# Kernel tuning notes

Hardware: AMD Instinct MI355X
Metric: run time of the kernel (lower is better)

Reference implementation:

```python
import jax, jax.numpy as jnp
import numpy as np

N = 4_194_304   # collocation points
H = 10          # num_neurons
L = 10          # num_layers (residual blocks)
DIN = 3         # (x, y, z) coords
DOUT = 1        # traveltime


def _linear_params(k, fan_in, fan_out, batch=()):
    # matches torch.nn.Linear default init: U(-1/sqrt(fan_in), 1/sqrt(fan_in))
    kw, kb = jax.random.split(k)
    s = 1.0 / np.sqrt(fan_in)
    W = jax.random.uniform(kw, batch + (fan_in, fan_out), minval=-s, maxval=s, dtype=jnp.float32)
    b = jax.random.uniform(kb, batch + (fan_out,), minval=-s, maxval=s, dtype=jnp.float32)
    return W, b


def setup_inputs() -> dict:
    key = jax.random.key(0)
    ks = jax.random.split(key, 8)
    x = jax.random.normal(ks[0], (N, DIN), dtype=jnp.float32)
    w0, b0 = _linear_params(ks[1], DIN, H)
    w1, b1 = _linear_params(ks[2], H, H)
    Wr1, Br1 = _linear_params(ks[3], H, H, (L,))
    Wr2, Br2 = _linear_params(ks[4], H, H, (L,))
    Wr3, Br3 = _linear_params(ks[5], H, H, (L,))
    w8, b8 = _linear_params(ks[6], H, H)
    w9, b9 = _linear_params(ks[7], H, DOUT)
    return dict(x=x, w0=w0, b0=b0, w1=w1, b1=b1,
                Wr1=Wr1, Br1=Br1, Wr2=Wr2, Br2=Br2, Wr3=Wr3, Br3=Br3,
                w8=w8, b8=b8, w9=w9, b9=b9)


def reference(x, w0, b0, w1, b1, Wr1, Br1, Wr2, Br2, Wr3, Br3, w8, b8, w9, b9):
    relu = jax.nn.relu
    h = relu(x @ w0 + b0)          # [N, H]
    h = relu(h @ w1 + b1)          # [N, H]

    def block(h, params):
        W1, B1, W2, B2, W3, B3 = params
        h1 = relu(h @ W1 + B1)
        h2 = relu(h1 @ W3 + B3 + h @ W2 + B2)  # residual mixing of x0 via W2
        return h2, None

    h, _ = jax.lax.scan(block, h, (Wr1, Br1, Wr2, Br2, Wr3, Br3))
    h = relu(h @ w8 + b8)
    out = h @ w9 + b9              # last_act=None, last_abs=False, last_multiplier=1
    return out
```

## Files before the change

### kernel.cpp

```cpp
#include <hip/hip_runtime.h>


#define NPTS 4194304
#define NBLK 2048
#define WPB 4
#define NWAVES (NBLK * WPB)
#define NTILES (NPTS / 32)
#define TPW (NTILES / NWAVES)
#define NMM 24
#define NLDS 20
#define ILP 2

typedef _Float16 h8 __attribute__((ext_vector_type(8)));
typedef float v16f __attribute__((ext_vector_type(16)));
typedef unsigned u4v __attribute__((ext_vector_type(4)));

__device__ __forceinline__ v16f mm(h8 a, h8 b, v16f c) {
    return __builtin_amdgcn_mfma_f32_32x32x16_f16(a, b, c, 0, 0, 0);
}
__device__ __forceinline__ unsigned pkrtz(float a, float b) {
    return __builtin_bit_cast(unsigned, __builtin_amdgcn_cvt_pkrtz(a, b));
}
__device__ __forceinline__ h8 relu8(h8 h) {
    h8 z = {0, 0, 0, 0, 0, 0, 0, 0};
    return __builtin_elementwise_max(h, z);
}
__device__ __forceinline__ h8 rc_lo(v16f d) {
    u4v u;
    u.x = pkrtz(d[0], d[1]); u.y = pkrtz(d[2], d[3]);
    u.z = pkrtz(d[4], d[5]); u.w = pkrtz(d[6], d[7]);
    return relu8(__builtin_bit_cast(h8, u));
}
__device__ __forceinline__ h8 rc_hi(v16f d) {
    u4v u;
    u.x = pkrtz(d[8], d[9]);   u.y = pkrtz(d[10], d[11]);
    u.z = pkrtz(d[12], d[13]); u.w = pkrtz(d[14], d[15]);
    return relu8(__builtin_bit_cast(h8, u));
}

__global__ __launch_bounds__(64) void prepack(
    const float* __restrict__ w0, const float* __restrict__ b0,
    const float* __restrict__ w1, const float* __restrict__ b1,
    const float* __restrict__ Wr1, const float* __restrict__ Br1,
    const float* __restrict__ Wr2, const float* __restrict__ Br2,
    const float* __restrict__ Wr3, const float* __restrict__ Br3,
    const float* __restrict__ w8, const float* __restrict__ b8,
    const float* __restrict__ w9, const float* __restrict__ b9,
    h8* __restrict__ tab)
{
    const int q = blockIdx.x, l = threadIdx.x;
    const int m = l & 31, g = l >> 5;
    h8 v;
#pragma unroll
    for (int j = 0; j < 8; ++j) {
        const int rr = (j & 3) + 8 * (j >> 2) + 4 * g;
        float a = 0.0f;
        if (q == 0) {
            if (m < 10 && rr < 3)        a = w0[rr * 10 + m];
            else if (m < 10 && rr == 3)  a = b0[m];
            else if (m == 10 && rr == 3) a = 1.0f;
        } else if (q == 1 || q == 22) {
            const float* W = (q == 1) ? w1 : w8;
            const float* B = (q == 1) ? b1 : b8;
            if (m < 10 && rr < 10)        a = W[rr * 10 + m];
            else if (m < 10 && rr == 10)  a = B[m];
            else if (m == 10 && rr == 10) a = 1.0f;
        } else if (q == 23) {
            if (m == 0 && rr < 10)       a = w9[rr];
            else if (m == 0 && rr == 10) a = b9[0];
        } else if (((q - 2) & 1) == 0) {
            const int bl = (q - 2) >> 1;
            if (m < 10) {
                if (rr < 10)       a = Wr1[bl * 100 + rr * 10 + m];
                else if (rr == 10) a = Br1[bl * 10 + m];
            } else if (m >= 16 && m < 26) {
                if (rr < 10)       a = Wr2[bl * 100 + rr * 10 + (m - 16)];
                else if (rr == 10) a = Br2[bl * 10 + (m - 16)] + Br3[bl * 10 + (m - 16)];
            } else if (m == 26 && rr == 10) {
                a = 1.0f;
            }
        } else {
            const int bl = (q - 3) >> 1;
            if (m >= 16 && m < 26 && rr < 10)
                a = Wr3[bl * 100 + rr * 10 + (m - 16)];
        }
        v[j] = (_Float16)a;
    }
    tab[q * 64 + l] = v;
}

__global__ __launch_bounds__(256, 6) void resnet_fwd(
    const float* __restrict__ x,
    const h8* __restrict__ tab,
    float* __restrict__ out)
{
    const int lane = threadIdx.x & 63;
    const int wv = blockIdx.x * WPB + (threadIdx.x >> 6);
    const int col = lane & 31;
    const bool lo = lane < 32;

    const h8 rA0 = tab[0 * 64 + lane];
    const h8 rA1 = tab[1 * 64 + lane];
    const h8 rA8 = tab[22 * 64 + lane];
    const h8 rA9 = tab[23 * 64 + lane];

    __shared__ h8 sA[NLDS * 64];
    for (int i = threadIdx.x; i < NLDS * 64; i += 256) sA[i] = tab[128 + i];
    __syncthreads();

    v16f zero;
#pragma unroll
    for (int j = 0; j < 16; ++j) zero[j] = 0.0f;
    asm volatile("" : "+v"(zero));

    const long p0 = (long)wv * TPW * 32;
    const float* px = x + (p0 + col) * 3;
    float* po = out + p0 + col;

    for (int t = 0; t < TPW; t += ILP) {
        int ln = lane;
        asm volatile("" : "+v"(ln));
        const h8* wp = &sA[ln];

        h8 hh[ILP];
#pragma unroll
        for (int c = 0; c < ILP; ++c) {
            float a0 = 0.f, a1 = 0.f, a2 = 0.f;
            if (lo) { a0 = px[c * 96 + 0]; a1 = px[c * 96 + 1];
                      a2 = px[c * 96 + 2]; }
            u4v u;
            u.x = pkrtz(a0, a1); u.y = pkrtz(a2, lo ? 1.0f : 0.0f);
            u.z = 0u; u.w = 0u;
            hh[c] = __builtin_bit_cast(h8, u);
        }

#pragma unroll
        for (int c = 0; c < ILP; ++c) hh[c] = rc_lo(mm(rA0, hh[c], zero));
#pragma unroll
        for (int c = 0; c < ILP; ++c) hh[c] = rc_lo(mm(rA1, hh[c], zero));

#pragma unroll
        for (int bl = 0; bl < 10; ++bl) {
            h8 a12 = wp[(2 * bl) * 64];
            h8 a3  = wp[(2 * bl + 1) * 64];
            v16f d12[ILP];
#pragma unroll
            for (int c = 0; c < ILP; ++c) d12[c] = mm(a12, hh[c], zero);
#pragma unroll
            for (int c = 0; c < ILP; ++c) {
                h8 t1 = rc_lo(d12[c]);
                d12[c] = mm(a3, t1, d12[c]);
            }
#pragma unroll
            for (int c = 0; c < ILP; ++c) hh[c] = rc_hi(d12[c]);
        }

#pragma unroll
        for (int c = 0; c < ILP; ++c) hh[c] = rc_lo(mm(rA8, hh[c], zero));

#pragma unroll
        for (int c = 0; c < ILP; ++c) {
            v16f d = mm(rA9, hh[c], zero);
            if (lo) po[c * 32] = d[0];
        }

        px += ILP * 96;
        po += ILP * 32;
    }
}

extern "C" void kernel_launch(void* const* d_in, const int* in_sizes, int n_in,
                              void* d_out, int out_size, void* d_ws, size_t ws_size,
                              hipStream_t stream)
{
    const float* x   = (const float*)d_in[0];
    const float* w0  = (const float*)d_in[1];
    const float* b0  = (const float*)d_in[2];
    const float* w1  = (const float*)d_in[3];
    const float* b1  = (const float*)d_in[4];
    const float* Wr1 = (const float*)d_in[5];
    const float* Br1 = (const float*)d_in[6];
    const float* Wr2 = (const float*)d_in[7];
    const float* Br2 = (const float*)d_in[8];
    const float* Wr3 = (const float*)d_in[9];
    const float* Br3 = (const float*)d_in[10];
    const float* w8  = (const float*)d_in[11];
    const float* b8  = (const float*)d_in[12];
    const float* w9  = (const float*)d_in[13];
    const float* b9  = (const float*)d_in[14];
    float* out = (float*)d_out;
    h8* tab = (h8*)d_ws;

    hipLaunchKernelGGL(prepack, dim3(NMM), dim3(64), 0, stream,
                       w0, b0, w1, b1, Wr1, Br1, Wr2, Br2, Wr3, Br3,
                       w8, b8, w9, b9, tab);

    hipLaunchKernelGGL(resnet_fwd, dim3(NBLK), dim3(256), 0, stream,
                       x, (const h8*)tab, out);
}
```

Baseline: 174.2 us.

## Hand-schedule MFMA chain in inline asm with four tiles and prefetch

Replaces the compiler-generated MFMA chain with a hand-written inline-assembly sequence that processes four 32-point tiles per iteration. All weight matrices live in LDS and are double-buffered with ds_read prefetches, hazards are covered by explicit s_nop padding, and the next chunk's inputs are loaded from global memory one iteration ahead. Occupancy drops to 3 blocks per CU in exchange for more independent MFMAs per wave. This hardcodes about 112 VGPRs and fixed nop counts, so it risks wasted cycles or hazards if the latency assumptions are wrong.

```diff
diff --git a/kernel.cpp b/kernel.cpp
--- a/kernel.cpp
+++ b/kernel.cpp
@@ -8,34 +8,12 @@
 #define NTILES (NPTS / 32)
 #define TPW (NTILES / NWAVES)
 #define NMM 24
-#define NLDS 20
-#define ILP 2
+#define CH 4
 
 typedef _Float16 h8 __attribute__((ext_vector_type(8)));
-typedef float v16f __attribute__((ext_vector_type(16)));
-typedef unsigned u4v __attribute__((ext_vector_type(4)));
-
-__device__ __forceinline__ v16f mm(h8 a, h8 b, v16f c) {
-    return __builtin_amdgcn_mfma_f32_32x32x16_f16(a, b, c, 0, 0, 0);
-}
+
 __device__ __forceinline__ unsigned pkrtz(float a, float b) {
     return __builtin_bit_cast(unsigned, __builtin_amdgcn_cvt_pkrtz(a, b));
-}
-__device__ __forceinline__ h8 relu8(h8 h) {
-    h8 z = {0, 0, 0, 0, 0, 0, 0, 0};
-    return __builtin_elementwise_max(h, z);
-}
-__device__ __forceinline__ h8 rc_lo(v16f d) {
-    u4v u;
-    u.x = pkrtz(d[0], d[1]); u.y = pkrtz(d[2], d[3]);
-    u.z = pkrtz(d[4], d[5]); u.w = pkrtz(d[6], d[7]);
-    return relu8(__builtin_bit_cast(h8, u));
-}
-__device__ __forceinline__ h8 rc_hi(v16f d) {
-    u4v u;
-    u.x = pkrtz(d[8], d[9]);   u.y = pkrtz(d[10], d[11]);
-    u.z = pkrtz(d[12], d[13]); u.w = pkrtz(d[14], d[15]);
-    return relu8(__builtin_bit_cast(h8, u));
 }
 
 __global__ __launch_bounds__(64) void prepack(
@@ -89,83 +67,255 @@
     tab[q * 64 + l] = v;
 }
 
-__global__ __launch_bounds__(256, 6) void resnet_fwd(
+
+#define MM4_Z(P) \
+  "v_mfma_f32_32x32x16_f16 v[32:47], " P ", v[96:99],   v[16:31]\n" \
+  "v_mfma_f32_32x32x16_f16 v[48:63], " P ", v[100:103], v[16:31]\n" \
+  "v_mfma_f32_32x32x16_f16 v[64:79], " P ", v[104:107], v[16:31]\n" \
+  "v_mfma_f32_32x32x16_f16 v[80:95], " P ", v[108:111], v[16:31]\n"
+
+#define MM4_ACC(P) \
+  "v_mfma_f32_32x32x16_f16 v[32:47], " P ", v[96:99],   v[32:47]\n" \
+  "v_mfma_f32_32x32x16_f16 v[48:63], " P ", v[100:103], v[48:63]\n" \
+  "v_mfma_f32_32x32x16_f16 v[64:79], " P ", v[104:107], v[64:79]\n" \
+  "v_mfma_f32_32x32x16_f16 v[80:95], " P ", v[108:111], v[80:95]\n"
+
+#define RCLO_ALL \
+  "v_cvt_pkrtz_f16_f32 v96,  v32, v33\n" \
+  "v_cvt_pkrtz_f16_f32 v97,  v34, v35\n" \
+  "v_cvt_pkrtz_f16_f32 v98,  v36, v37\n" \
+  "v_cvt_pkrtz_f16_f32 v99,  v38, v39\n" \
+  "v_pk_max_f16 v96, v96, 0\n" \
+  "v_pk_max_f16 v97, v97, 0\n" \
+  "v_pk_max_f16 v98, v98, 0\n" \
+  "v_pk_max_f16 v99, v99, 0\n" \
+  "v_cvt_pkrtz_f16_f32 v100, v48, v49\n" \
+  "v_cvt_pkrtz_f16_f32 v101, v50, v51\n" \
+  "v_cvt_pkrtz_f16_f32 v102, v52, v53\n" \
+  "v_cvt_pkrtz_f16_f32 v103, v54, v55\n" \
+  "v_pk_max_f16 v100, v100, 0\n" \
+  "v_pk_max_f16 v101, v101, 0\n" \
+  "v_pk_max_f16 v102, v102, 0\n" \
+  "v_pk_max_f16 v103, v103, 0\n" \
+  "v_cvt_pkrtz_f16_f32 v104, v64, v65\n" \
+  "v_cvt_pkrtz_f16_f32 v105, v66, v67\n" \
+  "v_cvt_pkrtz_f16_f32 v106, v68, v69\n" \
+  "v_cvt_pkrtz_f16_f32 v107, v70, v71\n" \
+  "v_pk_max_f16 v104, v104, 0\n" \
+  "v_pk_max_f16 v105, v105, 0\n" \
+  "v_pk_max_f16 v106, v106, 0\n" \
+  "v_pk_max_f16 v107, v107, 0\n" \
+  "v_cvt_pkrtz_f16_f32 v108, v80, v81\n" \
+  "v_cvt_pkrtz_f16_f32 v109, v82, v83\n" \
+  "v_cvt_pkrtz_f16_f32 v110, v84, v85\n" \
+  "v_cvt_pkrtz_f16_f32 v111, v86, v87\n" \
+  "v_pk_max_f16 v108, v108, 0\n" \
+  "v_pk_max_f16 v109, v109, 0\n" \
+  "v_pk_max_f16 v110, v110, 0\n" \
+  "v_pk_max_f16 v111, v111, 0\n"
+
+#define RCHI_ALL \
+  "v_cvt_pkrtz_f16_f32 v96,  v40, v41\n" \
+  "v_cvt_pkrtz_f16_f32 v97,  v42, v43\n" \
+  "v_cvt_pkrtz_f16_f32 v98,  v44, v45\n" \
+  "v_cvt_pkrtz_f16_f32 v99,  v46, v47\n" \
+  "v_pk_max_f16 v96, v96, 0\n" \
+  "v_pk_max_f16 v97, v97, 0\n" \
+  "v_pk_max_f16 v98, v98, 0\n" \
+  "v_pk_max_f16 v99, v99, 0\n" \
+  "v_cvt_pkrtz_f16_f32 v100, v56, v57\n" \
+  "v_cvt_pkrtz_f16_f32 v101, v58, v59\n" \
+  "v_cvt_pkrtz_f16_f32 v102, v60, v61\n" \
+  "v_cvt_pkrtz_f16_f32 v103, v62, v63\n" \
+  "v_pk_max_f16 v100, v100, 0\n" \
+  "v_pk_max_f16 v101, v101, 0\n" \
+  "v_pk_max_f16 v102, v102, 0\n" \
+  "v_pk_max_f16 v103, v103, 0\n" \
+  "v_cvt_pkrtz_f16_f32 v104, v72, v73\n" \
+  "v_cvt_pkrtz_f16_f32 v105, v74, v75\n" \
+  "v_cvt_pkrtz_f16_f32 v106, v76, v77\n" \
+  "v_cvt_pkrtz_f16_f32 v107, v78, v79\n" \
+  "v_pk_max_f16 v104, v104, 0\n" \
+  "v_pk_max_f16 v105, v105, 0\n" \
+  "v_pk_max_f16 v106, v106, 0\n" \
+  "v_pk_max_f16 v107, v107, 0\n" \
+  "v_cvt_pkrtz_f16_f32 v108, v88, v89\n" \
+  "v_cvt_pkrtz_f16_f32 v109, v90, v91\n" \
+  "v_cvt_pkrtz_f16_f32 v110, v92, v93\n" \
+  "v_cvt_pkrtz_f16_f32 v111, v94, v95\n" \
+  "v_pk_max_f16 v108, v108, 0\n" \
+  "v_pk_max_f16 v109, v109, 0\n" \
+  "v_pk_max_f16 v110, v110, 0\n" \
+  "v_pk_max_f16 v111, v111, 0\n"
+
+#define ST_BLOCK(P12, P3, F12, F3) \
+  "s_waitcnt lgkmcnt(2)\n" \
+  MM4_Z(P12) \
+  "s_nop 7\ns_nop 7\ns_nop 2\n" \
+  RCLO_ALL \
+  "s_nop 1\n" \
+  MM4_ACC(P3) \
+  "ds_read_b128 " P12 ", %[ad] offset:" F12 "\n" \
+  "ds_read_b128 " P3  ", %[ad] offset:" F3  "\n" \
+  "s_nop 7\ns_nop 6\n" \
+  RCHI_ALL \
+  "s_nop 1\n"
+
+#define ST_BLOCK_NOPF(P12, P3) \
+  "s_waitcnt lgkmcnt(2)\n" \
+  MM4_Z(P12) \
+  "s_nop 7\ns_nop 7\ns_nop 2\n" \
+  RCLO_ALL \
+  "s_nop 1\n" \
+  MM4_ACC(P3) \
+  "s_nop 7\ns_nop 7\ns_nop 2\n" \
+  RCHI_ALL \
+  "s_nop 1\n"
+
+#define ST_FIRST \
+  "s_waitcnt lgkmcnt(2)\n" \
+  MM4_Z("v[112:115]") \
+  "s_nop 7\ns_nop 7\ns_nop 2\n" \
+  RCLO_ALL \
+  "s_nop 1\n" \
+  MM4_Z("v[116:119]") \
+  "ds_read_b128 v[112:115], %[ad] offset:4096\n" \
+  "ds_read_b128 v[116:119], %[ad] offset:5120\n" \
+  "s_nop 7\ns_nop 6\n" \
+  RCLO_ALL \
+  "s_nop 1\n"
+
+#define ST_LAST \
+  "s_waitcnt lgkmcnt(0)\n" \
+  MM4_Z("v[120:123]") \
+  "s_nop 7\ns_nop 7\ns_nop 2\n" \
+  RCLO_ALL \
+  "s_nop 1\n" \
+  MM4_Z("v[124:127]") \
+  "s_nop 7\ns_nop 7\ns_nop 2\n" \
+  "v_mov_b32 %[o0], v32\n" \
+  "v_mov_b32 %[o1], v48\n" \
+  "v_mov_b32 %[o2], v64\n" \
+  "v_mov_b32 %[o3], v80\n"
+
+#define PROLOG \
+  "v_mov_b32 v16, 0\n" "v_mov_b32 v17, 0\n" "v_mov_b32 v18, 0\n" "v_mov_b32 v19, 0\n" \
+  "v_mov_b32 v20, 0\n" "v_mov_b32 v21, 0\n" "v_mov_b32 v22, 0\n" "v_mov_b32 v23, 0\n" \
+  "v_mov_b32 v24, 0\n" "v_mov_b32 v25, 0\n" "v_mov_b32 v26, 0\n" "v_mov_b32 v27, 0\n" \
+  "v_mov_b32 v28, 0\n" "v_mov_b32 v29, 0\n" "v_mov_b32 v30, 0\n" "v_mov_b32 v31, 0\n" \
+  "v_mov_b32 v96,  %[g0]\n" "v_mov_b32 v97,  %[g1]\n" \
+  "v_mov_b32 v98,  0\n"     "v_mov_b32 v99,  0\n" \
+  "v_mov_b32 v100, %[g2]\n" "v_mov_b32 v101, %[g3]\n" \
+  "v_mov_b32 v102, 0\n"     "v_mov_b32 v103, 0\n" \
+  "v_mov_b32 v104, %[g4]\n" "v_mov_b32 v105, %[g5]\n" \
+  "v_mov_b32 v106, 0\n"     "v_mov_b32 v107, 0\n" \
+  "v_mov_b32 v108, %[g6]\n" "v_mov_b32 v109, %[g7]\n" \
+  "v_mov_b32 v110, 0\n"     "v_mov_b32 v111, 0\n" \
+  "ds_read_b128 v[112:115], %[ad] offset:0\n" \
+  "ds_read_b128 v[116:119], %[ad] offset:1024\n" \
+  "ds_read_b128 v[120:123], %[ad] offset:2048\n" \
+  "ds_read_b128 v[124:127], %[ad] offset:3072\n"
+
+#define CHAIN_ASM \
+  PROLOG \
+  ST_FIRST \
+  ST_BLOCK("v[120:123]", "v[124:127]",  "6144",  "7168") \
+  ST_BLOCK("v[112:115]", "v[116:119]",  "8192",  "9216") \
+  ST_BLOCK("v[120:123]", "v[124:127]", "10240", "11264") \
+  ST_BLOCK("v[112:115]", "v[116:119]", "12288", "13312") \
+  ST_BLOCK("v[120:123]", "v[124:127]", "14336", "15360") \
+  ST_BLOCK("v[112:115]", "v[116:119]", "16384", "17408") \
+  ST_BLOCK("v[120:123]", "v[124:127]", "18432", "19456") \
+  ST_BLOCK("v[112:115]", "v[116:119]", "20480", "21504") \
+  ST_BLOCK("v[120:123]", "v[124:127]", "22528", "23552") \
+  ST_BLOCK_NOPF("v[112:115]", "v[116:119]") \
+  ST_LAST
+
+#define VCLOB \
+  "v16","v17","v18","v19","v20","v21","v22","v23", \
+  "v24","v25","v26","v27","v28","v29","v30","v31", \
+  "v32","v33","v34","v35","v36","v37","v38","v39", \
+  "v40","v41","v42","v43","v44","v45","v46","v47", \
+  "v48","v49","v50","v51","v52","v53","v54","v55", \
+  "v56","v57","v58","v59","v60","v61","v62","v63", \
+  "v64","v65","v66","v67","v68","v69","v70","v71", \
+  "v72","v73","v74","v75","v76","v77","v78","v79", \
+  "v80","v81","v82","v83","v84","v85","v86","v87", \
+  "v88","v89","v90","v91","v92","v93","v94","v95", \
+  "v96","v97","v98","v99","v100","v101","v102","v103", \
+  "v104","v105","v106","v107","v108","v109","v110","v111", \
+  "v112","v113","v114","v115","v116","v117","v118","v119", \
+  "v120","v121","v122","v123","v124","v125","v126","v127"
+
+__global__ __launch_bounds__(256, 3) void resnet_fwd(
     const float* __restrict__ x,
     const h8* __restrict__ tab,
     float* __restrict__ out)
 {
+    __shared__ h8 sA[NMM * 64];
+    for (int i = threadIdx.x; i < NMM * 64; i += 256) sA[i] = tab[i];
+    __syncthreads();
+
     const int lane = threadIdx.x & 63;
     const int wv = blockIdx.x * WPB + (threadIdx.x >> 6);
     const int col = lane & 31;
     const bool lo = lane < 32;
-
-    const h8 rA0 = tab[0 * 64 + lane];
-    const h8 rA1 = tab[1 * 64 + lane];
-    const h8 rA8 = tab[22 * 64 + lane];
-    const h8 rA9 = tab[23 * 64 + lane];
-
-    __shared__ h8 sA[NLDS * 64];
-    for (int i = threadIdx.x; i < NLDS * 64; i += 256) sA[i] = tab[128 + i];
-    __syncthreads();
-
-    v16f zero;
-#pragma unroll
-    for (int j = 0; j < 16; ++j) zero[j] = 0.0f;
-    asm volatile("" : "+v"(zero));
+    const float m = lo ? 1.0f : 0.0f;
+
+    const unsigned ad = (unsigned)(size_t)(&sA[lane]);
 
     const long p0 = (long)wv * TPW * 32;
     const float* px = x + (p0 + col) * 3;
     float* po = out + p0 + col;
 
-    for (int t = 0; t < TPW; t += ILP) {
-        int ln = lane;
-        asm volatile("" : "+v"(ln));
-        const h8* wp = &sA[ln];
-
-        h8 hh[ILP];
-#pragma unroll
-        for (int c = 0; c < ILP; ++c) {
-            float a0 = 0.f, a1 = 0.f, a2 = 0.f;
-            if (lo) { a0 = px[c * 96 + 0]; a1 = px[c * 96 + 1];
-                      a2 = px[c * 96 + 2]; }
-            u4v u;
-            u.x = pkrtz(a0, a1); u.y = pkrtz(a2, lo ? 1.0f : 0.0f);
-            u.z = 0u; u.w = 0u;
-            hh[c] = __builtin_bit_cast(h8, u);
+    float xa[CH * 3];
+#pragma unroll
+    for (int c = 0; c < CH; ++c) {
+        xa[c * 3 + 0] = px[c * 96 + 0];
+        xa[c * 3 + 1] = px[c * 96 + 1];
+        xa[c * 3 + 2] = px[c * 96 + 2];
+    }
+
+#pragma unroll 1
+    for (int t = 0; t < TPW; t += CH) {
+        unsigned g[2 * CH];
+#pragma unroll
+        for (int c = 0; c < CH; ++c) {
+            float a0 = lo ? xa[c * 3 + 0] : 0.0f;
+            float a1 = lo ? xa[c * 3 + 1] : 0.0f;
+            float a2 = lo ? xa[c * 3 + 2] : 0.0f;
+            g[2 * c + 0] = pkrtz(a0, a1);
+            g[2 * c + 1] = pkrtz(a2, m);
         }
 
-#pragma unroll
-        for (int c = 0; c < ILP; ++c) hh[c] = rc_lo(mm(rA0, hh[c], zero));
-#pragma unroll
-        for (int c = 0; c < ILP; ++c) hh[c] = rc_lo(mm(rA1, hh[c], zero));
-
-#pragma unroll
-        for (int bl = 0; bl < 10; ++bl) {
-            h8 a12 = wp[(2 * bl) * 64];
-            h8 a3  = wp[(2 * bl + 1) * 64];
-            v16f d12[ILP];
-#pragma unroll
-            for (int c = 0; c < ILP; ++c) d12[c] = mm(a12, hh[c], zero);
-#pragma unroll
-            for (int c = 0; c < ILP; ++c) {
-                h8 t1 = rc_lo(d12[c]);
-                d12[c] = mm(a3, t1, d12[c]);
+        const float* pn = px + CH * 96;
+        float nx[CH * 3];
+#pragma unroll
+        for (int i = 0; i < CH * 3; ++i) nx[i] = 0.0f;
+        if (t + CH < TPW) {
+#pragma unroll
+            for (int c = 0; c < CH; ++c) {
+                nx[c * 3 + 0] = pn[c * 96 + 0];
+                nx[c * 3 + 1] = pn[c * 96 + 1];
+                nx[c * 3 + 2] = pn[c * 96 + 2];
             }
-#pragma unroll
-            for (int c = 0; c < ILP; ++c) hh[c] = rc_hi(d12[c]);
         }
 
-#pragma unroll
-        for (int c = 0; c < ILP; ++c) hh[c] = rc_lo(mm(rA8, hh[c], zero));
-
-#pragma unroll
-        for (int c = 0; c < ILP; ++c) {
-            v16f d = mm(rA9, hh[c], zero);
-            if (lo) po[c * 32] = d[0];
-        }
-
-        px += ILP * 96;
-        po += ILP * 32;
+        float o0, o1, o2, o3;
+        asm volatile(
+            CHAIN_ASM
+            : [o0] "=v"(o0), [o1] "=v"(o1), [o2] "=v"(o2), [o3] "=v"(o3)
+            : [g0] "v"(g[0]), [g1] "v"(g[1]), [g2] "v"(g[2]), [g3] "v"(g[3]),
+              [g4] "v"(g[4]), [g5] "v"(g[5]), [g6] "v"(g[6]), [g7] "v"(g[7]),
+              [ad] "v"(ad)
+            : VCLOB);
+
+        if (lo) { po[0] = o0; po[32] = o1; po[64] = o2; po[96] = o3; }
+
+        px = pn;
+        po += CH * 32;
+#pragma unroll
+        for (int i = 0; i < CH * 3; ++i) xa[i] = nx[i];
     }
 }
 
```

New measurement: 175.0 us. No clear change (+0.4%).
